# Optimization experiments

Hardware: AMD Instinct MI355X
Metric: run time of the kernel (lower is better)

## Reference

```python
import jax, jax.numpy as jnp
import numpy as np

ALPHA = 2.0      # spikingjelly surrogate.ATan default alpha
TAU_LIF = 2.0    # LIFNode tau
V_TH = 1.0       # spike threshold (v_reset = 0.0, hard reset)


@jax.custom_vjp
def spike_fn(x):
    # Heaviside forward (spikingjelly: x >= 0 -> 1)
    return (x >= 0.0).astype(x.dtype)

def _spike_fwd(x):
    return spike_fn(x), x

def _spike_bwd(x, g):
    # ATan surrogate gradient: alpha/2 / (1 + (pi/2 * alpha * x)^2)
    return (g * (ALPHA / 2.0) / (1.0 + (jnp.pi / 2.0 * ALPHA * x) ** 2),)

spike_fn.defvjp(_spike_fwd, _spike_bwd)


def setup_inputs() -> dict:
    key = jax.random.key(0)
    ks = jax.random.split(key, 5)
    B, T, I, H, O = 256, 1000, 700, 64, 20
    x = jax.random.normal(ks[0], (B, T, I), dtype=jnp.float32)
    W_h = jax.random.normal(ks[1], (H, I), dtype=jnp.float32) / np.sqrt(I).astype(np.float32)
    b_h = jnp.zeros((H,), dtype=jnp.float32)
    W_r = jax.random.normal(ks[2], (O, H), dtype=jnp.float32) / np.sqrt(H).astype(np.float32)
    b_r = jnp.zeros((O,), dtype=jnp.float32)
    tau_m = jax.random.uniform(ks[3], (O,), dtype=jnp.float32, minval=0.0, maxval=4.0)
    return {"x": x, "W_h": W_h, "b_h": b_h, "W_r": W_r, "b_r": b_r, "tau_m": tau_m}


def reference(x, W_h, b_h, W_r, b_r, tau_m):
    B, T, I = x.shape
    H = W_h.shape[0]
    O = W_r.shape[0]
    # One big GEMM for all hidden input currents: [T, B, H]
    currents = jnp.einsum('bti,hi->tbh', x, W_h) + b_h
    beta = jax.nn.sigmoid(tau_m)  # readout leak [O]
    # original accumulates softmax only for t > 10
    mask = (jnp.arange(T) > 10).astype(x.dtype)

    def step(carry, inp):
        v, v_ro, acc = carry
        cur, m = inp
        # LIF charge (decay_input=True, v_reset=0): v += (cur - v)/tau
        v = v + (cur - v) / TAU_LIF
        s = spike_fn(v - V_TH)
        # hard reset to v_reset = 0
        v = v * (1.0 - s)
        # readout leaky integrator
        ro_in = s @ W_r.T + b_r                      # [B, O]
        v_ro = v_ro * beta + (1.0 - beta) * ro_in
        acc = acc + m * jax.nn.softmax(v_ro, axis=-1)
        return (v, v_ro, acc), None

    init = (jnp.zeros((B, H), x.dtype),
            jnp.zeros((B, O), x.dtype),
            jnp.zeros((B, O), x.dtype))
    (_, _, acc), _ = jax.lax.scan(step, init, (currents, mask))
    return acc
```

## Files before the change

### kernel.cpp

```cpp
#include <hip/hip_runtime.h>


typedef float  f32x4  __attribute__((ext_vector_type(4)));
typedef short  short8 __attribute__((ext_vector_type(8)));
typedef unsigned long long ull;

#define B_   256
#define T_   1000
#define K_   700
#define H_   64
#define O_   20
#define NKT  11
#define NMT  8
#define NCH  200
#define TCH  5

#define OFF_WFRAG  ((size_t)0)

__global__ void wprep(const float* __restrict__ Wh, unsigned short* __restrict__ wfrag) {
    int e = blockIdx.x * 256 + threadIdx.x;
    int kt   = e >> 9;
    int rem  = e & 511;
    int nf   = rem >> 7;
    int kf   = (rem >> 6) & 1;
    int lane = rem & 63;
    int h     = nf * 16 + (lane & 15);
    int kbase = kt * 64 + kf * 32 + ((lane >> 4) & 3) * 8;
    int slot  = (nf * 2 + kf) * 64 + lane;
    unsigned short* dh = wfrag + (size_t)kt * 8192 + slot * 8;
    unsigned short* dl = dh + 4096;
#pragma unroll
    for (int j = 0; j < 8; ++j) {
        int k = kbase + j;
        float v = (k < K_) ? Wh[(size_t)h * K_ + k] : 0.0f;
        unsigned u  = __builtin_bit_cast(unsigned, v);
        float    fh = __builtin_bit_cast(float, u & 0xffff0000u);
        float    r  = v - fh;
        dh[j] = (unsigned short)(u >> 16);
        dl[j] = (unsigned short)(__builtin_bit_cast(unsigned, r) >> 16);
    }
}

__device__ __forceinline__ void glds16(const void* src, void* lds) {
    __builtin_amdgcn_global_load_lds(
        (const __attribute__((address_space(1))) void*)src,
        (__attribute__((address_space(3))) void*)lds, 16, 0, 0);
}

__device__ __forceinline__ void splitpair(f32x4 p0, f32x4 p1, short8& hi, short8& lo) {
#pragma unroll
    for (int j = 0; j < 4; ++j) {
        {
            unsigned u  = __builtin_bit_cast(unsigned, p0[j]);
            float    fh = __builtin_bit_cast(float, u & 0xffff0000u);
            float    r  = p0[j] - fh;
            hi[j] = (short)(u >> 16);
            lo[j] = (short)(__builtin_bit_cast(unsigned, r) >> 16);
        }
        {
            unsigned u  = __builtin_bit_cast(unsigned, p1[j]);
            float    fh = __builtin_bit_cast(float, u & 0xffff0000u);
            float    r  = p1[j] - fh;
            hi[j + 4] = (short)(u >> 16);
            lo[j + 4] = (short)(__builtin_bit_cast(unsigned, r) >> 16);
        }
    }
}

__device__ __forceinline__ void stage_x(const float* __restrict__ x, size_t brow0,
                                        int mt, int kt, int tid, float* sbuf) {
#pragma unroll
    for (int j = 0; j < 4; ++j) {
        int id = j * 512 + tid;
        int s2 = id >> 10;
        int r  = (id >> 3) & 127;
        int pc = id & 7;
        int c  = pc ^ (r & 7);
        int trow = mt * 128 + r;
        if (trow >= T_) trow = 0;
        int kbyte = kt * 256 + s2 * 128 + (c << 4);
        if (kbyte + 16 > K_ * 4) kbyte = 0;
        const char* src = (const char*)(x + (brow0 + trow) * (size_t)K_) + kbyte;
        float* dst = sbuf + (size_t)(id & ~63) * 4;
        glds16(src, dst);
    }
}

__device__ __forceinline__ void stage_w(const unsigned short* __restrict__ wfrag,
                                        int kt, int tid, unsigned short* sbuf) {
#pragma unroll
    for (int j = 0; j < 2; ++j) {
        int id = j * 512 + tid;
        const unsigned short* src = wfrag + (size_t)kt * 8192 + id * 8;
        unsigned short* dst = sbuf + (size_t)(id & ~63) * 8;
        glds16(src, dst);
    }
}

__device__ __forceinline__ void compute128(const float* sbx_, const unsigned short* sbw_,
                                           int lane, int wid, f32x4 (&acc)[4]) {
    const char*   xb = (const char*)sbx_;
    const short8* wb = (const short8*)sbw_;
    int rloc = wid * 16 + (lane & 15);
    int g2   = ((lane >> 4) & 3) * 2;
#pragma unroll
    for (int kf = 0; kf < 2; ++kf) {
        const char* base = xb + kf * 16384 + rloc * 128;
        int c0 = g2 ^ (rloc & 7);
        int c1 = (g2 + 1) ^ (rloc & 7);
        f32x4 p0 = *(const f32x4*)(base + c0 * 16);
        f32x4 p1 = *(const f32x4*)(base + c1 * 16);
        short8 ah, al;
        splitpair(p0, p1, ah, al);
#pragma unroll
        for (int n = 0; n < 4; ++n) {
            short8 bhf = wb[(n * 2 + kf) * 64 + lane];
            short8 blf = wb[(n * 2 + kf) * 64 + lane + 512];
            acc[n] = __builtin_amdgcn_mfma_f32_16x16x32_bf16(ah, bhf, acc[n], 0, 0, 0);
            acc[n] = __builtin_amdgcn_mfma_f32_16x16x32_bf16(al, bhf, acc[n], 0, 0, 0);
            acc[n] = __builtin_amdgcn_mfma_f32_16x16x32_bf16(ah, blf, acc[n], 0, 0, 0);
        }
    }
}

__global__ __launch_bounds__(512, 2) void fused(const float* __restrict__ x,
                                                const unsigned short* __restrict__ wfrag,
                                                const float* __restrict__ b_h,
                                                const float* __restrict__ Wr,
                                                const float* __restrict__ br,
                                                const float* __restrict__ tau,
                                                float* __restrict__ out) {
    __shared__ __align__(16) char  pool[98304];
    __shared__ __align__(16) float curT[128 * 64];
    __shared__ ull smaskL[T_];

    int tid  = threadIdx.x;
    int lane = tid & 63;
    int wid  = tid >> 6;
    int b    = blockIdx.x;
    size_t brow0 = (size_t)b * T_;

    float*          sbx0 = (float*)pool;
    float*          sbx1 = (float*)(pool + 32768);
    unsigned short* sbw0 = (unsigned short*)(pool + 65536);
    unsigned short* sbw1 = (unsigned short*)(pool + 81920);

    float bh4[4];
#pragma unroll
    for (int n = 0; n < 4; ++n) bh4[n] = b_h[n * 16 + (lane & 15)];

    f32x4 acc[4];
#pragma unroll
    for (int n = 0; n < 4; ++n) acc[n] = (f32x4){0.f, 0.f, 0.f, 0.f};
    float v = 0.0f;

    stage_x(x, brow0, 0, 0, tid, sbx0);  stage_w(wfrag, 0, tid, sbw0);
    stage_x(x, brow0, 0, 1, tid, sbx1);  stage_w(wfrag, 1, tid, sbw1);

    int p = 0;
    for (int mt = 0; mt < NMT; ++mt) {
#pragma unroll
        for (int kt = 0; kt <= 10; ++kt) {
            float*          xb = p ? sbx1 : sbx0;
            unsigned short* wb = p ? sbw1 : sbw0;
            if (kt == 10 && mt == NMT - 1) {
                asm volatile("s_waitcnt vmcnt(0)" ::: "memory");
            } else {
                asm volatile("s_waitcnt vmcnt(6)" ::: "memory");
            }
            __builtin_amdgcn_s_barrier();
            compute128(xb, wb, lane, wid, acc);
            if (kt == 10) {
#pragma unroll
                for (int n = 0; n < 4; ++n) {
#pragma unroll
                    for (int j = 0; j < 4; ++j) {
                        int tloc = wid * 16 + ((lane >> 4) & 3) * 4 + j;
                        curT[tloc * 64 + n * 16 + (lane & 15)] = acc[n][j] + bh4[n];
                    }
                    acc[n] = (f32x4){0.f, 0.f, 0.f, 0.f};
                }
            }
            asm volatile("s_waitcnt lgkmcnt(0)" ::: "memory");
            __builtin_amdgcn_s_barrier();
            int smt = mt, skt = kt + 2;
            if (skt >= NKT) { smt += 1; skt -= NKT; }
            if (smt < NMT) {
                stage_x(x, brow0, smt, skt, tid, xb);
                stage_w(wfrag, skt, tid, wb);
            }
            p ^= 1;
            if (kt == 10) {
                int tcnt = T_ - mt * 128; if (tcnt > 128) tcnt = 128;
                for (int j = 0; j < tcnt; ++j) {
                    float c = curT[j * 64 + lane];
                    v = (v + c) * 0.5f;
                    bool sp = (v >= 1.0f);
                    ull m = __ballot(sp);
                    if (wid == (j >> 4) && lane == 0) smaskL[mt * 128 + j] = m;
                    v = sp ? 0.0f : v;
                }
            }
        }
    }
    __syncthreads();

    float* wt     = (float*)pool;
    float (*E)[20]    = (float(*)[20])(pool + 5120);
    float (*Sv)[20]   = (float(*)[20])(pool + 21120);
    float (*pacc)[20] = (float(*)[20])(pool + 37120);
    float* sScale = (float*)(pool + 53120);
    float* sBase  = (float*)(pool + 53216);
    float* sBeta  = (float*)(pool + 53312);
    float (*Pg)[20]   = (float(*)[20])(pool + 53408);
    float (*Sst)[20]  = (float(*)[20])(pool + 54048);
    float (*part)[20] = (float(*)[20])(pool + 54688);

    for (int i = tid; i < 1280; i += 512) wt[(i & 63) * 20 + (i >> 6)] = Wr[(size_t)(i >> 6) * 64 + (i & 63)];
    if (tid < 20) {
        float beta = 1.0f / (1.0f + __expf(-tau[tid]));
        sBeta[tid]  = beta;
        sScale[tid] = 1.0f - beta;
        sBase[tid]  = br[tid];
    }
    __syncthreads();

    for (int it = tid; it < NCH * 5; it += 512) {
        int o4 = it % 5;
        int c  = it / 5;
        f32x4 beta4  = *(const f32x4*)&sBeta[o4 * 4];
        f32x4 scale4 = *(const f32x4*)&sScale[o4 * 4];
        f32x4 base4  = *(const f32x4*)&sBase[o4 * 4];
        f32x4 vv = {0.f, 0.f, 0.f, 0.f};
        const ull* mp = smaskL + c * TCH;
#pragma unroll
        for (int j = 0; j < TCH; ++j) {
            ull m = mp[j];
            f32x4 a = {0.f, 0.f, 0.f, 0.f};
            while (m) {
                int h = __builtin_ctzll(m);
                m &= (m - 1);
                a += *(const f32x4*)&wt[h * 20 + o4 * 4];
            }
            f32x4 q;
#pragma unroll
            for (int jj = 0; jj < 4; ++jj) q[jj] = scale4[jj] * (base4[jj] + a[jj]);
            vv = beta4 * vv + q;
        }
        *(f32x4*)&E[c][o4 * 4] = vv;
    }
    __syncthreads();

    if (tid < 160) {
        int o = tid >> 3, g = tid & 7;
        float beta = sBeta[o];
        float b2 = beta * beta;
        float bp = b2 * b2 * beta;
        float P = 0.0f;
        for (int c = g * 25; c < g * 25 + 25; ++c) P = bp * P + E[c][o];
        Pg[g][o] = P;
    }
    __syncthreads();

    if (tid < 20) {
        int o = tid;
        float beta = sBeta[o];
        float b2 = beta * beta;
        float bp = b2 * b2 * beta;
        float bp25 = 1.0f;
#pragma unroll
        for (int i = 0; i < 25; ++i) bp25 *= bp;
        float s = 0.0f;
        for (int g = 0; g < 8; ++g) { Sst[g][o] = s; s = bp25 * s + Pg[g][o]; }
    }
    __syncthreads();

    if (tid < 160) {
        int o = tid >> 3, g = tid & 7;
        float beta = sBeta[o];
        float b2 = beta * beta;
        float bp = b2 * b2 * beta;
        float s = Sst[g][o];
        for (int c = g * 25; c < g * 25 + 25; ++c) { Sv[c][o] = s; s = bp * s + E[c][o]; }
    }
    __syncthreads();

    if (tid < NCH) {
        int c = tid;
        float beta[20], vv[20], ac[20];
#pragma unroll
        for (int o = 0; o < 20; ++o) {
            beta[o] = sBeta[o];
            vv[o]  = Sv[c][o];
            ac[o]  = 0.0f;
        }
        int t0 = c * TCH;
        const ull* mp = smaskL + t0;
#pragma unroll
        for (int j = 0; j < TCH; ++j) {
            int t = t0 + j;
            ull m = mp[j];
            f32x4 a[5];
#pragma unroll
            for (int i = 0; i < 5; ++i) a[i] = (f32x4){0.f, 0.f, 0.f, 0.f};
            while (m) {
                int h = __builtin_ctzll(m);
                m &= (m - 1);
                const f32x4* w4 = (const f32x4*)&wt[h * 20];
#pragma unroll
                for (int i = 0; i < 5; ++i) a[i] += w4[i];
            }
#pragma unroll
            for (int o = 0; o < 20; ++o) {
                float q = sScale[o] * (sBase[o] + a[o >> 2][o & 3]);
                vv[o] = beta[o] * vv[o] + q;
            }
            if (t >= 11) {
                float mx = vv[0];
#pragma unroll
                for (int o = 1; o < 20; ++o) mx = fmaxf(mx, vv[o]);
                float e[20], ssum = 0.0f;
#pragma unroll
                for (int o = 0; o < 20; ++o) { e[o] = __expf(vv[o] - mx); ssum += e[o]; }
                float inv = 1.0f / ssum;
#pragma unroll
                for (int o = 0; o < 20; ++o) ac[o] += e[o] * inv;
            }
        }
#pragma unroll
        for (int o = 0; o < 20; ++o) pacc[c][o] = ac[o];
    }
    __syncthreads();

    if (tid < 160) {
        int o = tid >> 3, g = tid & 7;
        float s = 0.0f;
        for (int c = g * 25; c < g * 25 + 25; ++c) s += pacc[c][o];
        part[g][o] = s;
    }
    __syncthreads();
    if (tid < 20) {
        float s = 0.0f;
#pragma unroll
        for (int g = 0; g < 8; ++g) s += part[g][tid];
        out[(size_t)b * 20 + tid] = s;
    }
}

extern "C" void kernel_launch(void* const* d_in, const int* in_sizes, int n_in,
                              void* d_out, int out_size, void* d_ws, size_t ws_size,
                              hipStream_t stream) {
    const float* x   = (const float*)d_in[0];
    const float* W_h = (const float*)d_in[1];
    const float* b_h = (const float*)d_in[2];
    const float* W_r = (const float*)d_in[3];
    const float* b_r = (const float*)d_in[4];
    const float* tau = (const float*)d_in[5];

    char* ws = (char*)d_ws;
    unsigned short* wfrag = (unsigned short*)(ws + OFF_WFRAG);
    float* out = (float*)d_out;

    wprep<<<22, 256, 0, stream>>>(W_h, wfrag);
    fused<<<B_, 512, 0, stream>>>(x, wfrag, b_h, W_r, b_r, tau, out);
}
```

Baseline: 219.9 us.

## Keep W_h fragments in registers and stream 32-row x tiles in halves

The fused kernel now loads the whole bf16 hi/lo split of W_h into registers once per wave, which removes per-step LDS staging of the weights. The x tile shrinks from 128 rows by 64 k to 32 full rows, split into two half-K pieces and staged through a triple-buffered LDS ring. The 8 waves become a 2x4 grid over rows and hidden columns, each holding one accumulator. The LIF scan runs every 32 timesteps instead of every 128, interleaved with the staging. The cost is heavy register pressure (44 short8 weight values), more barriers per timestep, and LDS use of about 150KB, which likely cuts occupancy to one block per CU.

New measurement: 285.7 us. +29.9%, slower.

```diff
diff --git a/kernel.cpp b/kernel.cpp
--- a/kernel.cpp
+++ b/kernel.cpp
@@ -10,25 +10,25 @@
 #define K_   700
 #define H_   64
 #define O_   20
-#define NKT  11
-#define NMT  8
 #define NCH  200
 #define TCH  5
 
-#define OFF_WFRAG  ((size_t)0)
+#define L_XBUF   45056
+#define L_SCR    135168
+#define L_CURT   136192
+#define L_MASK   144384
+#define L_TOT    152384
 
 __global__ void wprep(const float* __restrict__ Wh, unsigned short* __restrict__ wfrag) {
     int e = blockIdx.x * 256 + threadIdx.x;
-    int kt   = e >> 9;
-    int rem  = e & 511;
-    int nf   = rem >> 7;
-    int kf   = (rem >> 6) & 1;
+    int kt   = e >> 8;
+    int rem  = e & 255;
+    int nf   = rem >> 6;
     int lane = rem & 63;
     int h     = nf * 16 + (lane & 15);
-    int kbase = kt * 64 + kf * 32 + ((lane >> 4) & 3) * 8;
-    int slot  = (nf * 2 + kf) * 64 + lane;
-    unsigned short* dh = wfrag + (size_t)kt * 8192 + slot * 8;
-    unsigned short* dl = dh + 4096;
+    int kbase = kt * 32 + ((lane >> 4) & 3) * 8;
+    unsigned short* dh = wfrag + (size_t)kt * 4096 + (nf * 64 + lane) * 8;
+    unsigned short* dl = dh + 2048;
 #pragma unroll
     for (int j = 0; j < 8; ++j) {
         int k = kbase + j;
@@ -67,59 +67,22 @@
     }
 }
 
-__device__ __forceinline__ void stage_x(const float* __restrict__ x, size_t brow0,
-                                        int mt, int kt, int tid, float* sbuf) {
-#pragma unroll
-    for (int j = 0; j < 4; ++j) {
-        int id = j * 512 + tid;
-        int s2 = id >> 10;
-        int r  = (id >> 3) & 127;
-        int pc = id & 7;
-        int c  = pc ^ (r & 7);
-        int trow = mt * 128 + r;
-        if (trow >= T_) trow = 0;
-        int kbyte = kt * 256 + s2 * 128 + (c << 4);
-        if (kbyte + 16 > K_ * 4) kbyte = 0;
-        const char* src = (const char*)(x + (brow0 + trow) * (size_t)K_) + kbyte;
-        float* dst = sbuf + (size_t)(id & ~63) * 4;
-        glds16(src, dst);
-    }
-}
-
-__device__ __forceinline__ void stage_w(const unsigned short* __restrict__ wfrag,
-                                        int kt, int tid, unsigned short* sbuf) {
-#pragma unroll
-    for (int j = 0; j < 2; ++j) {
-        int id = j * 512 + tid;
-        const unsigned short* src = wfrag + (size_t)kt * 8192 + id * 8;
-        unsigned short* dst = sbuf + (size_t)(id & ~63) * 8;
-        glds16(src, dst);
-    }
-}
-
-__device__ __forceinline__ void compute128(const float* sbx_, const unsigned short* sbw_,
-                                           int lane, int wid, f32x4 (&acc)[4]) {
-    const char*   xb = (const char*)sbx_;
-    const short8* wb = (const short8*)sbw_;
-    int rloc = wid * 16 + (lane & 15);
-    int g2   = ((lane >> 4) & 3) * 2;
-#pragma unroll
-    for (int kf = 0; kf < 2; ++kf) {
-        const char* base = xb + kf * 16384 + rloc * 128;
-        int c0 = g2 ^ (rloc & 7);
-        int c1 = (g2 + 1) ^ (rloc & 7);
-        f32x4 p0 = *(const f32x4*)(base + c0 * 16);
-        f32x4 p1 = *(const f32x4*)(base + c1 * 16);
-        short8 ah, al;
-        splitpair(p0, p1, ah, al);
-#pragma unroll
-        for (int n = 0; n < 4; ++n) {
-            short8 bhf = wb[(n * 2 + kf) * 64 + lane];
-            short8 blf = wb[(n * 2 + kf) * 64 + lane + 512];
-            acc[n] = __builtin_amdgcn_mfma_f32_16x16x32_bf16(ah, bhf, acc[n], 0, 0, 0);
-            acc[n] = __builtin_amdgcn_mfma_f32_16x16x32_bf16(al, bhf, acc[n], 0, 0, 0);
-            acc[n] = __builtin_amdgcn_mfma_f32_16x16x32_bf16(ah, blf, acc[n], 0, 0, 0);
-        }
+__device__ __forceinline__ void stage_piece(const char* xb, int g, int h,
+                                            char* dstbase, char* scratch, int wid,
+                                            const int (&pr)[6], const int (&pco0)[6],
+                                            const int (&pco1)[6], const int (&pd)[6]) {
+#pragma unroll
+    for (int j = 0; j < 5; ++j) {
+        int row = g * 32 + pr[j]; row = row > (T_ - 1) ? (T_ - 1) : row;
+        int co  = h ? pco1[j] : pco0[j];
+        glds16(xb + (size_t)row * 2800 + h * 1408 + co, dstbase + pd[j]);
+    }
+    if (wid < 4) {
+        int row = g * 32 + pr[5]; row = row > (T_ - 1) ? (T_ - 1) : row;
+        int co  = h ? pco1[5] : pco0[5];
+        glds16(xb + (size_t)row * 2800 + h * 1408 + co, dstbase + pd[5]);
+    } else {
+        glds16(xb, scratch);
     }
 }
 
@@ -130,81 +93,120 @@
                                                 const float* __restrict__ br,
                                                 const float* __restrict__ tau,
                                                 float* __restrict__ out) {
-    __shared__ __align__(16) char  pool[98304];
-    __shared__ __align__(16) float curT[128 * 64];
-    __shared__ ull smaskL[T_];
+    __shared__ __align__(16) char L[L_TOT];
 
     int tid  = threadIdx.x;
     int lane = tid & 63;
     int wid  = tid >> 6;
+    int wm   = wid >> 2;
+    int wn   = wid & 3;
     int b    = blockIdx.x;
-    size_t brow0 = (size_t)b * T_;
-
-    float*          sbx0 = (float*)pool;
-    float*          sbx1 = (float*)(pool + 32768);
-    unsigned short* sbw0 = (unsigned short*)(pool + 65536);
-    unsigned short* sbw1 = (unsigned short*)(pool + 81920);
-
-    float bh4[4];
-#pragma unroll
-    for (int n = 0; n < 4; ++n) bh4[n] = b_h[n * 16 + (lane & 15)];
-
-    f32x4 acc[4];
-#pragma unroll
-    for (int n = 0; n < 4; ++n) acc[n] = (f32x4){0.f, 0.f, 0.f, 0.f};
+    const char* xb = (const char*)x + (size_t)b * T_ * K_ * 4;
+
+    float* curTf = (float*)(L + L_CURT);
+    ull*   maskp = (ull*)(L + L_MASK);
+    char*  scr   = L + L_SCR;
+
+    short8 wHi[22], wLo[22];
+#pragma unroll
+    for (int kt = 0; kt < 22; ++kt) {
+        const short8* base = (const short8*)(wfrag + (size_t)kt * 4096);
+        wHi[kt] = base[wn * 64 + lane];
+        wLo[kt] = base[256 + wn * 64 + lane];
+    }
+    float bh = b_h[wn * 16 + (lane & 15)];
+    asm volatile("s_waitcnt vmcnt(0)" ::: "memory");
+
+    int pr[6], pco0[6], pco1[6], pd[6];
+#pragma unroll
+    for (int j = 0; j < 6; ++j) {
+        int id, dst;
+        if (j < 5) { id = (wid + 8 * j) * 64 + lane; dst = (wid + 8 * j) * 1024; }
+        else       { id = 2560 + wid * 64 + lane;    dst = 40960 + wid * 1024; }
+        int r  = id / 88;
+        int pc = id - r * 88;
+        int c  = pc ^ (r & 7);
+        pr[j]   = r;
+        pco0[j] = c * 16;
+        pco1[j] = (c == 87 ? 86 : c) * 16;
+        pd[j]   = dst;
+    }
+
+    int rr = wm * 16 + (lane & 15);
+    int rx = rr & 7;
+    int g2 = ((lane >> 4) & 3) * 2;
+
+    f32x4 acc = {0.f, 0.f, 0.f, 0.f};
     float v = 0.0f;
 
-    stage_x(x, brow0, 0, 0, tid, sbx0);  stage_w(wfrag, 0, tid, sbw0);
-    stage_x(x, brow0, 0, 1, tid, sbx1);  stage_w(wfrag, 1, tid, sbw1);
-
-    int p = 0;
-    for (int mt = 0; mt < NMT; ++mt) {
-#pragma unroll
-        for (int kt = 0; kt <= 10; ++kt) {
-            float*          xb = p ? sbx1 : sbx0;
-            unsigned short* wb = p ? sbw1 : sbw0;
-            if (kt == 10 && mt == NMT - 1) {
-                asm volatile("s_waitcnt vmcnt(0)" ::: "memory");
-            } else {
-                asm volatile("s_waitcnt vmcnt(6)" ::: "memory");
-            }
-            __builtin_amdgcn_s_barrier();
-            compute128(xb, wb, lane, wid, acc);
-            if (kt == 10) {
-#pragma unroll
-                for (int n = 0; n < 4; ++n) {
-#pragma unroll
-                    for (int j = 0; j < 4; ++j) {
-                        int tloc = wid * 16 + ((lane >> 4) & 3) * 4 + j;
-                        curT[tloc * 64 + n * 16 + (lane & 15)] = acc[n][j] + bh4[n];
-                    }
-                    acc[n] = (f32x4){0.f, 0.f, 0.f, 0.f};
-                }
-            }
-            asm volatile("s_waitcnt lgkmcnt(0)" ::: "memory");
-            __builtin_amdgcn_s_barrier();
-            int smt = mt, skt = kt + 2;
-            if (skt >= NKT) { smt += 1; skt -= NKT; }
-            if (smt < NMT) {
-                stage_x(x, brow0, smt, skt, tid, xb);
-                stage_w(wfrag, skt, tid, wb);
-            }
-            p ^= 1;
-            if (kt == 10) {
-                int tcnt = T_ - mt * 128; if (tcnt > 128) tcnt = 128;
-                for (int j = 0; j < tcnt; ++j) {
-                    float c = curT[j * 64 + lane];
-                    v = (v + c) * 0.5f;
-                    bool sp = (v >= 1.0f);
-                    ull m = __ballot(sp);
-                    if (wid == (j >> 4) && lane == 0) smaskL[mt * 128 + j] = m;
-                    v = sp ? 0.0f : v;
-                }
-            }
-        }
-    }
-    __syncthreads();
-
+    stage_piece(xb, 0, 0, L + 0 * L_XBUF, scr, wid, pr, pco0, pco1, pd);
+    stage_piece(xb, 0, 1, L + 1 * L_XBUF, scr, wid, pr, pco0, pco1, pd);
+    stage_piece(xb, 1, 0, L + 2 * L_XBUF, scr, wid, pr, pco0, pco1, pd);
+
+#define COMPUTE_HALF(H, BUF)                                                  \
+    {                                                                         \
+        const char* xr = L + (BUF) * L_XBUF + rr * 1408;                      \
+        _Pragma("unroll")                                                     \
+        for (int kt = 0; kt < 11; ++kt) {                                     \
+            int pcb = kt * 8 + g2;                                            \
+            f32x4 p0 = *(const f32x4*)(xr + ((pcb) ^ rx) * 16);               \
+            f32x4 p1 = *(const f32x4*)(xr + ((pcb + 1) ^ rx) * 16);           \
+            short8 ah, al;                                                    \
+            splitpair(p0, p1, ah, al);                                        \
+            acc = __builtin_amdgcn_mfma_f32_16x16x32_bf16(ah, wHi[(H)*11+kt], acc, 0, 0, 0); \
+            acc = __builtin_amdgcn_mfma_f32_16x16x32_bf16(al, wHi[(H)*11+kt], acc, 0, 0, 0); \
+            acc = __builtin_amdgcn_mfma_f32_16x16x32_bf16(ah, wLo[(H)*11+kt], acc, 0, 0, 0); \
+        }                                                                     \
+    }
+
+#define GROUP_BODY(VMA, VMB, DO_S1, DO_S2)                                    \
+    {                                                                         \
+        asm volatile("s_waitcnt vmcnt(" VMA ")" ::: "memory");                \
+        __builtin_amdgcn_s_barrier();                                         \
+        COMPUTE_HALF(0, ba)                                                   \
+        asm volatile("s_waitcnt lgkmcnt(0)" ::: "memory");                    \
+        __builtin_amdgcn_s_barrier();                                         \
+        if (DO_S1) stage_piece(xb, g + 1, 1, L + ba * L_XBUF, scr, wid, pr, pco0, pco1, pd); \
+        asm volatile("s_waitcnt vmcnt(" VMB ")" ::: "memory");                \
+        __builtin_amdgcn_s_barrier();                                         \
+        COMPUTE_HALF(1, bb)                                                   \
+        _Pragma("unroll")                                                     \
+        for (int j = 0; j < 4; ++j) {                                         \
+            int tt = wm * 16 + ((lane >> 4) & 3) * 4 + j;                     \
+            curTf[tt * 64 + wn * 16 + (lane & 15)] = acc[j] + bh;             \
+        }                                                                     \
+        acc = (f32x4){0.f, 0.f, 0.f, 0.f};                                    \
+        asm volatile("s_waitcnt lgkmcnt(0)" ::: "memory");                    \
+        __builtin_amdgcn_s_barrier();                                         \
+        if (DO_S2) stage_piece(xb, g + 2, 0, L + bb * L_XBUF, scr, wid, pr, pco0, pco1, pd); \
+        {                                                                     \
+            int tcnt = T_ - g * 32; if (tcnt > 32) tcnt = 32;                 \
+            for (int j = 0; j < tcnt; ++j) {                                  \
+                float c = curTf[j * 64 + lane];                               \
+                v = (v + c) * 0.5f;                                           \
+                bool sp = (v >= 1.0f);                                        \
+                ull m = __ballot(sp);                                         \
+                if (tid == 0) maskp[g * 32 + j] = m;                          \
+                v = sp ? 0.0f : v;                                            \
+            }                                                                 \
+        }                                                                     \
+    }
+
+    int ba = 0, bb = 1;
+    for (int g = 0; g < 31; ++g) {
+        GROUP_BODY("12", "12", true, (g < 30))
+        ba += 2; if (ba >= 3) ba -= 3;
+        bb += 2; if (bb >= 3) bb -= 3;
+    }
+    {
+        int g = 31;
+        GROUP_BODY("6", "0", false, false)
+    }
+#undef GROUP_BODY
+#undef COMPUTE_HALF
+    __syncthreads();
+
+    char* pool = L;
     float* wt     = (float*)pool;
     float (*E)[20]    = (float(*)[20])(pool + 5120);
     float (*Sv)[20]   = (float(*)[20])(pool + 21120);
@@ -215,6 +217,7 @@
     float (*Pg)[20]   = (float(*)[20])(pool + 53408);
     float (*Sst)[20]  = (float(*)[20])(pool + 54048);
     float (*part)[20] = (float(*)[20])(pool + 54688);
+    const ull* smaskL = (const ull*)(L + L_MASK);
 
     for (int i = tid; i < 1280; i += 512) wt[(i & 63) * 20 + (i >> 6)] = Wr[(size_t)(i >> 6) * 64 + (i & 63)];
     if (tid < 20) {
@@ -357,8 +360,7 @@
     const float* b_r = (const float*)d_in[4];
     const float* tau = (const float*)d_in[5];
 
-    char* ws = (char*)d_ws;
-    unsigned short* wfrag = (unsigned short*)(ws + OFF_WFRAG);
+    unsigned short* wfrag = (unsigned short*)d_ws;
     float* out = (float*)d_out;
 
     wprep<<<22, 256, 0, stream>>>(W_h, wfrag);
```
